# Optimization experiments

Measured on AMD Instinct MI355X. Metric: run time of the kernel, lower is better.

## Reference

```python
import jax, jax.numpy as jnp
import numpy as np
from jax import lax

HEAD_NUM = 16
QKV_DIM = 16
TOP_K = 2
SQRT_EMBED = 16.0   # sqrt_embedding_dim for E=256
LOGIT_CLIP = 10.0


def setup_inputs() -> dict:
    key = jax.random.key(0)
    ks = jax.random.split(key, 12)
    B, P, N1, E, HD, NE = 256, 100, 101, 256, 256, 8
    s = 0.05
    return {
        "encoded_last_node": jax.random.normal(ks[0], (B, P, E), jnp.float32),
        "attr": jax.random.uniform(ks[1], (B, P, 4), jnp.float32),
        "encoded_nodes": jax.random.normal(ks[2], (B, N1, E), jnp.float32),
        "ninf_mask": jnp.zeros((B, P, N1), jnp.float32),
        "attention_bias": jax.random.normal(ks[3], (B, P, N1), jnp.float32),
        "attention_bias1": jax.random.normal(ks[4], (B, P, N1), jnp.float32),
        "Wq_last": jax.random.normal(ks[5], (E + 4, HD), jnp.float32) * s,
        "Wk": jax.random.normal(ks[6], (E, HD), jnp.float32) * s,
        "Wv": jax.random.normal(ks[7], (E, HD), jnp.float32) * s,
        "Wg": jax.random.normal(ks[8], (HD, NE), jnp.float32) * s,
        "expert_W": jax.random.normal(ks[9], (NE, HD, E), jnp.float32) * s,
        "expert_b": jnp.zeros((NE, E), jnp.float32),
    }


def _heads(x, H, D):
    B, n, _ = x.shape
    return x.reshape(B, n, H, D).transpose(0, 2, 1, 3)  # (B,H,n,D)


def reference(encoded_last_node, attr, encoded_nodes, ninf_mask,
              attention_bias, attention_bias1, Wq_last, Wk, Wv,
              Wg, expert_W, expert_b):
    B, P, E = encoded_last_node.shape
    H, D = HEAD_NUM, QKV_DIM
    # q from [last_node ; attr], k/v from encoded_nodes (set_kv)
    q = _heads(jnp.concatenate([encoded_last_node, attr], axis=-1) @ Wq_last, H, D)
    k = _heads(encoded_nodes @ Wk, H, D)   # (B,H,N+1,D)
    v = _heads(encoded_nodes @ Wv, H, D)
    inv_sqrt_d = 1.0 / jnp.sqrt(jnp.asarray(D, jnp.float32))
    score = jnp.einsum('bhpd,bhnd->bhpn', q, k) * inv_sqrt_d
    score = score + ninf_mask[:, None, :, :]           # rank3 ninf mask
    w = jax.nn.softmax(score, axis=-1)
    out = jnp.einsum('bhpn,bhnd->bhpd', w, v)
    out_concat = out.transpose(0, 2, 1, 3).reshape(B, P, H * D)
    # --- top-k gated MoE combine (node-level routing, eval path) ---
    x = out_concat.reshape(B * P, H * D)               # tokens
    logits = x @ Wg                                    # (T, NE)
    top_v, top_i = lax.top_k(logits, TOP_K)
    top_g = jax.nn.softmax(top_v, axis=-1)
    gates = jnp.zeros_like(logits).at[
        jnp.arange(x.shape[0])[:, None], top_i].set(top_g)   # (T, NE)
    expert_out = jnp.einsum('tf,efo->teo', x, expert_W) + expert_b[None]
    mh = jnp.einsum('teo,te->to', expert_out, gates).reshape(B, P, E)
    # --- single-head pointer scores with bias + tanh clipping ---
    score2 = jnp.einsum('bpe,bne->bpn', mh, encoded_nodes)
    score2 = score2 + attention_bias + attention_bias1
    score2 = LOGIT_CLIP * jnp.tanh(score2 / SQRT_EMBED)
    probs = jax.nn.softmax(score2 + ninf_mask, axis=-1)  # (B,P,N+1)
    return probs
```

## Files before the change

kernel.cpp:

```cpp
#include <hip/hip_runtime.h>
#include <hip/hip_bf16.h>

#define B   256
#define P   100
#define N1  101
#define E   256
#define HD  256
#define H   16
#define D   16
#define NE  8
#define NTOK (B*P)
#define NKV  (B*N1)

typedef __attribute__((ext_vector_type(8))) short short8;
typedef __attribute__((ext_vector_type(4))) float f32x4;
typedef unsigned short ushort_t;

__device__ __forceinline__ unsigned short f2bf(float f) {
  unsigned int u = __float_as_uint(f);
  unsigned int r = (u + 0x7fffu + ((u >> 16) & 1u)) >> 16;
  return (unsigned short)r;
}
__device__ __forceinline__ float bf2f(unsigned short b) {
  return __uint_as_float(((unsigned int)b) << 16);
}
__device__ __forceinline__ unsigned int cvtpk(float a, float b) {
  unsigned int r;
  asm("v_cvt_pk_bf16_f32 %0, %1, %2" : "=v"(r) : "v"(a), "v"(b));
  return r;
}
__device__ __forceinline__ float lo2f(unsigned int u) {
  return __uint_as_float(u << 16);
}
__device__ __forceinline__ float hi2f(unsigned int u) {
  return __uint_as_float(u & 0xffff0000u);
}

__device__ __forceinline__ void split3_pack(const float* v, uint4& uh,
                                            uint4& um, uint4& ul) {
  unsigned int hw[4], mw[4], lw[4];
#pragma unroll
  for (int jj = 0; jj < 4; ++jj) {
    float va = v[2 * jj], vb = v[2 * jj + 1];
    unsigned int h = cvtpk(va, vb);
    float ra = va - lo2f(h), rb = vb - hi2f(h);
    unsigned int m = cvtpk(ra, rb);
    float sa = ra - lo2f(m), sb = rb - hi2f(m);
    unsigned int l = cvtpk(sa, sb);
    hw[jj] = h; mw[jj] = m; lw[jj] = l;
  }
  uh.x = hw[0]; uh.y = hw[1]; uh.z = hw[2]; uh.w = hw[3];
  um.x = mw[0]; um.y = mw[1]; um.z = mw[2]; um.w = mw[3];
  ul.x = lw[0]; ul.y = lw[1]; ul.z = lw[2]; ul.w = lw[3];
}

__global__ __launch_bounds__(256) void wsplit3_kernel(
    const float* __restrict__ W, uint4* __restrict__ Wp, int Kreal) {
  const int gid = blockIdx.x * 256 + threadIdx.x;
  const int lane = gid & 63;
  const int rest = gid >> 6;
  const int gct = rest & 15;
  const int kt = rest >> 4;
  const int k0 = kt * 32 + (lane >> 4) * 8;
  const int c = gct * 16 + (lane & 15);
  float v[8];
#pragma unroll
  for (int j = 0; j < 8; ++j) {
    int kk = k0 + j;
    v[j] = (kk < Kreal) ? W[(size_t)kk * 256 + c] : 0.f;
  }
  uint4 uh, um, ul;
  split3_pack(v, uh, um, ul);
  Wp[(size_t)(rest * 3 + 0) * 64 + lane] = uh;
  Wp[(size_t)(rest * 3 + 1) * 64 + lane] = um;
  Wp[(size_t)(rest * 3 + 2) * 64 + lane] = ul;
}

__global__ __launch_bounds__(256) void kvproj3_kernel(
    const float* __restrict__ enc, const uint4* __restrict__ Wk3,
    const uint4* __restrict__ Wv3, float* __restrict__ kout,
    float* __restrict__ vout) {
  const int KT = 8;
  const int NKG = KT * 4;
  const int RSTRIDE = KT * 12 + 1;
  __shared__ uint4 als[32 * 97];
  const int tid = threadIdx.x;
  const int row0 = blockIdx.x * 32;
  for (int i = tid; i < 32 * NKG; i += 256) {
    const int row = i >> 5;
    const int kg = i & 31;
    float v[8];
    const float4* s = (const float4*)(enc + (size_t)(row0 + row) * 256 + kg * 8);
    float4 x0 = s[0], x1 = s[1];
    v[0] = x0.x; v[1] = x0.y; v[2] = x0.z; v[3] = x0.w;
    v[4] = x1.x; v[5] = x1.y; v[6] = x1.z; v[7] = x1.w;
    uint4 uh, um, ul;
    split3_pack(v, uh, um, ul);
    const int slot = row * RSTRIDE + kg;
    als[slot] = uh;
    als[slot + NKG] = um;
    als[slot + 2 * NKG] = ul;
  }
  __syncthreads();
  const int w = tid >> 6;
  const int lane = tid & 63;
  const int lr = lane & 15;
  const int lg4 = lane >> 4;
  f32x4 acck[2][4], accv[2][4];
#pragma unroll
  for (int rt = 0; rt < 2; ++rt)
#pragma unroll
    for (int ct = 0; ct < 4; ++ct) {
      acck[rt][ct] = (f32x4){0.f, 0.f, 0.f, 0.f};
      accv[rt][ct] = (f32x4){0.f, 0.f, 0.f, 0.f};
    }
  for (int kt = 0; kt < KT; ++kt) {
    short8 ah[2], am[2], al[2];
#pragma unroll
    for (int rt = 0; rt < 2; ++rt) {
      const int base = (rt * 16 + lr) * RSTRIDE + kt * 4 + lg4;
      ah[rt] = __builtin_bit_cast(short8, als[base]);
      am[rt] = __builtin_bit_cast(short8, als[base + NKG]);
      al[rt] = __builtin_bit_cast(short8, als[base + 2 * NKG]);
    }
#pragma unroll
    for (int ct = 0; ct < 4; ++ct) {
      const int gct = w * 4 + ct;
      const size_t base = (size_t)((kt * 16 + gct) * 3) * 64 + lane;
      {
        short8 bh = __builtin_bit_cast(short8, Wk3[base]);
        short8 bm = __builtin_bit_cast(short8, Wk3[base + 64]);
        short8 bl = __builtin_bit_cast(short8, Wk3[base + 128]);
#pragma unroll
        for (int rt = 0; rt < 2; ++rt) {
          f32x4 a = acck[rt][ct];
          a = __builtin_amdgcn_mfma_f32_16x16x32_bf16(ah[rt], bh, a, 0, 0, 0);
          a = __builtin_amdgcn_mfma_f32_16x16x32_bf16(ah[rt], bm, a, 0, 0, 0);
          a = __builtin_amdgcn_mfma_f32_16x16x32_bf16(am[rt], bh, a, 0, 0, 0);
          a = __builtin_amdgcn_mfma_f32_16x16x32_bf16(am[rt], bm, a, 0, 0, 0);
          a = __builtin_amdgcn_mfma_f32_16x16x32_bf16(ah[rt], bl, a, 0, 0, 0);
          a = __builtin_amdgcn_mfma_f32_16x16x32_bf16(al[rt], bh, a, 0, 0, 0);
          acck[rt][ct] = a;
        }
      }
      {
        short8 bh = __builtin_bit_cast(short8, Wv3[base]);
        short8 bm = __builtin_bit_cast(short8, Wv3[base + 64]);
        short8 bl = __builtin_bit_cast(short8, Wv3[base + 128]);
#pragma unroll
        for (int rt = 0; rt < 2; ++rt) {
          f32x4 a = accv[rt][ct];
          a = __builtin_amdgcn_mfma_f32_16x16x32_bf16(ah[rt], bh, a, 0, 0, 0);
          a = __builtin_amdgcn_mfma_f32_16x16x32_bf16(ah[rt], bm, a, 0, 0, 0);
          a = __builtin_amdgcn_mfma_f32_16x16x32_bf16(am[rt], bh, a, 0, 0, 0);
          a = __builtin_amdgcn_mfma_f32_16x16x32_bf16(am[rt], bm, a, 0, 0, 0);
          a = __builtin_amdgcn_mfma_f32_16x16x32_bf16(ah[rt], bl, a, 0, 0, 0);
          a = __builtin_amdgcn_mfma_f32_16x16x32_bf16(al[rt], bh, a, 0, 0, 0);
          accv[rt][ct] = a;
        }
      }
    }
  }
#pragma unroll
  for (int rt = 0; rt < 2; ++rt) {
#pragma unroll
    for (int ct = 0; ct < 4; ++ct) {
      const int gct = w * 4 + ct;
#pragma unroll
      for (int reg = 0; reg < 4; ++reg) {
        const int row = row0 + rt * 16 + lg4 * 4 + reg;
        int bb = row / N1, nn = row - bb * N1;
        size_t o = (((size_t)bb * H + gct) * N1 + nn) * D + lr;
        kout[o] = acck[rt][ct][reg];
        vout[o] = accv[rt][ct][reg];
      }
    }
  }
}

template <int KT, int MODE>
__global__ __launch_bounds__(256) void proj3_kernel(
    const float* __restrict__ src, const float* __restrict__ attr,
    const uint4* __restrict__ Wp3, float* __restrict__ outp) {
  const int RSTRIDE = KT * 12 + 1;
  __shared__ uint4 als[32 * (KT * 12 + 1)];
  const int tid = threadIdx.x;
  const int row0 = blockIdx.x * 32;
  const int NKG = KT * 4;
  for (int i = tid; i < 32 * NKG; i += 256) {
    const int row = i / NKG;
    const int kg = i - row * NKG;
    float v[8];
    const int kbase = kg * 8;
    if (MODE == 0 || kbase < 256) {
      const float4* s = (const float4*)(src + (size_t)(row0 + row) * 256 + kbase);
      float4 x0 = s[0], x1 = s[1];
      v[0] = x0.x; v[1] = x0.y; v[2] = x0.z; v[3] = x0.w;
      v[4] = x1.x; v[5] = x1.y; v[6] = x1.z; v[7] = x1.w;
    } else {
#pragma unroll
      for (int j = 0; j < 8; ++j) {
        int k = kbase + j;
        v[j] = (k >= 256 && k < 260) ? attr[(size_t)(row0 + row) * 4 + (k - 256)]
                                     : 0.f;
      }
    }
    uint4 uh, um, ul;
    split3_pack(v, uh, um, ul);
    const int slot = row * RSTRIDE + kg;
    als[slot] = uh;
    als[slot + NKG] = um;
    als[slot + 2 * NKG] = ul;
  }
  __syncthreads();
  const int w = tid >> 6;
  const int lane = tid & 63;
  const int lr = lane & 15;
  const int lg4 = lane >> 4;
  f32x4 acc[2][4];
#pragma unroll
  for (int rt = 0; rt < 2; ++rt)
#pragma unroll
    for (int ct = 0; ct < 4; ++ct) acc[rt][ct] = (f32x4){0.f, 0.f, 0.f, 0.f};
  for (int kt = 0; kt < KT; ++kt) {
    short8 ah[2], am[2], al[2];
#pragma unroll
    for (int rt = 0; rt < 2; ++rt) {
      const int base = (rt * 16 + lr) * RSTRIDE + kt * 4 + lg4;
      ah[rt] = __builtin_bit_cast(short8, als[base]);
      am[rt] = __builtin_bit_cast(short8, als[base + NKG]);
      al[rt] = __builtin_bit_cast(short8, als[base + 2 * NKG]);
    }
#pragma unroll
    for (int ct = 0; ct < 4; ++ct) {
      const int gct = w * 4 + ct;
      const size_t base = (size_t)((kt * 16 + gct) * 3) * 64 + lane;
      short8 bh = __builtin_bit_cast(short8, Wp3[base]);
      short8 bm = __builtin_bit_cast(short8, Wp3[base + 64]);
      short8 bl = __builtin_bit_cast(short8, Wp3[base + 128]);
#pragma unroll
      for (int rt = 0; rt < 2; ++rt) {
        f32x4 a = acc[rt][ct];
        a = __builtin_amdgcn_mfma_f32_16x16x32_bf16(ah[rt], bh, a, 0, 0, 0);
        a = __builtin_amdgcn_mfma_f32_16x16x32_bf16(ah[rt], bm, a, 0, 0, 0);
        a = __builtin_amdgcn_mfma_f32_16x16x32_bf16(am[rt], bh, a, 0, 0, 0);
        a = __builtin_amdgcn_mfma_f32_16x16x32_bf16(am[rt], bm, a, 0, 0, 0);
        a = __builtin_amdgcn_mfma_f32_16x16x32_bf16(ah[rt], bl, a, 0, 0, 0);
        a = __builtin_amdgcn_mfma_f32_16x16x32_bf16(al[rt], bh, a, 0, 0, 0);
        acc[rt][ct] = a;
      }
    }
  }
#pragma unroll
  for (int rt = 0; rt < 2; ++rt) {
#pragma unroll
    for (int ct = 0; ct < 4; ++ct) {
      const int gct = w * 4 + ct;
#pragma unroll
      for (int reg = 0; reg < 4; ++reg) {
        const int row = row0 + rt * 16 + lg4 * 4 + reg;
        size_t o;
        if (MODE == 0) {
          int bb = row / N1, nn = row - bb * N1;
          o = (((size_t)bb * H + gct) * N1 + nn) * D + lr;
        } else {
          int bb = row / P, pp = row - bb * P;
          o = (((size_t)bb * H + gct) * P + pp) * D + lr;
        }
        outp[o] = acc[rt][ct][reg];
      }
    }
  }
}

__device__ __forceinline__ float dot16f(
    const float4& a0, const float4& a1, const float4& a2, const float4& a3,
    const float4& b0, const float4& b1, const float4& b2, const float4& b3) {
  float s = a0.x * b0.x;
  s = fmaf(a0.y, b0.y, s); s = fmaf(a0.z, b0.z, s); s = fmaf(a0.w, b0.w, s);
  s = fmaf(a1.x, b1.x, s); s = fmaf(a1.y, b1.y, s); s = fmaf(a1.z, b1.z, s);
  s = fmaf(a1.w, b1.w, s);
  s = fmaf(a2.x, b2.x, s); s = fmaf(a2.y, b2.y, s); s = fmaf(a2.z, b2.z, s);
  s = fmaf(a2.w, b2.w, s);
  s = fmaf(a3.x, b3.x, s); s = fmaf(a3.y, b3.y, s); s = fmaf(a3.z, b3.z, s);
  s = fmaf(a3.w, b3.w, s);
  return s;
}

__global__ __launch_bounds__(256) void attn_kernel(
    const float* __restrict__ q, const float* __restrict__ k,
    const float* __restrict__ v, const float* __restrict__ ninf,
    float* __restrict__ x) {
  const int b = blockIdx.x >> 3;
  const int h0 = (blockIdx.x & 7) * 2;
  __shared__ float4 kl4[2 * N1 * 4];
  __shared__ float4 vl4[2 * N1 * 4];
  const int tid = threadIdx.x;
  {
    const float4* ks = (const float4*)(k + ((size_t)b * H + h0) * N1 * D);
    const float4* vs = (const float4*)(v + ((size_t)b * H + h0) * N1 * D);
    for (int i = tid; i < 2 * N1 * 4; i += 256) {
      kl4[i] = ks[i];
      vl4[i] = vs[i];
    }
  }
  const int w = tid >> 6;
  const int lane = tid & 63;
  const int hh = w >> 1;
  const int h = h0 + hh;
  const int prow = (w & 1) * 64 + lane;
  const bool act = (prow < P);
  const int p = act ? prow : (P - 1);
  const float LOG2E = 1.4426950408889634f;
  const float c1 = 0.25f * LOG2E;
  const float* qb = q + (((size_t)b * H + h) * P + p) * D;
  float4 qa0 = *(const float4*)&qb[0];
  float4 qa1 = *(const float4*)&qb[4];
  float4 qa2 = *(const float4*)&qb[8];
  float4 qa3 = *(const float4*)&qb[12];
  qa0.x *= c1; qa0.y *= c1; qa0.z *= c1; qa0.w *= c1;
  qa1.x *= c1; qa1.y *= c1; qa1.z *= c1; qa1.w *= c1;
  qa2.x *= c1; qa2.y *= c1; qa2.z *= c1; qa2.w *= c1;
  qa3.x *= c1; qa3.y *= c1; qa3.z *= c1; qa3.w *= c1;
  const float* mrow = ninf + ((size_t)b * P + p) * N1;
  const float* kw = (const float*)(kl4 + hh * N1 * 4);
  const float* vw = (const float*)(vl4 + hh * N1 * 4);
  __syncthreads();

  float m2 = -1e30f, l = 0.f;
  float o[16];
#pragma unroll
  for (int d = 0; d < 16; ++d) o[d] = 0.f;
  float4 mk = *(const float4*)&mrow[0];
  const float tmask = mrow[100];

  for (int it = 0; it < 25; ++it) {
    const int j = it * 4;
    const int nn = (it < 24) ? (j + 4) : 0;
    float4 nx = *(const float4*)&mrow[nn];
    const float4* kr0 = (const float4*)&kw[(j + 0) * D];
    const float4* kr1 = (const float4*)&kw[(j + 1) * D];
    const float4* kr2 = (const float4*)&kw[(j + 2) * D];
    const float4* kr3 = (const float4*)&kw[(j + 3) * D];
    float4 k00 = kr0[0], k01 = kr0[1], k02 = kr0[2], k03 = kr0[3];
    float4 k10 = kr1[0], k11 = kr1[1], k12 = kr1[2], k13 = kr1[3];
    float4 k20 = kr2[0], k21 = kr2[1], k22 = kr2[2], k23 = kr2[3];
    float4 k30 = kr3[0], k31 = kr3[1], k32 = kr3[2], k33 = kr3[3];
    float s0 = fmaf(mk.x, LOG2E, dot16f(qa0, qa1, qa2, qa3, k00, k01, k02, k03));
    float s1 = fmaf(mk.y, LOG2E, dot16f(qa0, qa1, qa2, qa3, k10, k11, k12, k13));
    float s2 = fmaf(mk.z, LOG2E, dot16f(qa0, qa1, qa2, qa3, k20, k21, k22, k23));
    float s3 = fmaf(mk.w, LOG2E, dot16f(qa0, qa1, qa2, qa3, k30, k31, k32, k33));
    float mn = fmaxf(fmaxf(fmaxf(s0, s1), fmaxf(s2, s3)), m2);
    float sc = exp2f(m2 - mn);
    float p0 = exp2f(s0 - mn), p1 = exp2f(s1 - mn);
    float p2 = exp2f(s2 - mn), p3 = exp2f(s3 - mn);
    l = fmaf(l, sc, (p0 + p1) + (p2 + p3));
    const float4* vr0 = (const float4*)&vw[(j + 0) * D];
    const float4* vr1 = (const float4*)&vw[(j + 1) * D];
    const float4* vr2 = (const float4*)&vw[(j + 2) * D];
    const float4* vr3 = (const float4*)&vw[(j + 3) * D];
#pragma unroll
    for (int dq = 0; dq < 4; ++dq) {
      float4 v0 = vr0[dq], v1 = vr1[dq], v2 = vr2[dq], v3 = vr3[dq];
      o[4 * dq + 0] = fmaf(o[4 * dq + 0], sc,
          fmaf(p0, v0.x, fmaf(p1, v1.x, fmaf(p2, v2.x, p3 * v3.x))));
      o[4 * dq + 1] = fmaf(o[4 * dq + 1], sc,
          fmaf(p0, v0.y, fmaf(p1, v1.y, fmaf(p2, v2.y, p3 * v3.y))));
      o[4 * dq + 2] = fmaf(o[4 * dq + 2], sc,
          fmaf(p0, v0.z, fmaf(p1, v1.z, fmaf(p2, v2.z, p3 * v3.z))));
      o[4 * dq + 3] = fmaf(o[4 * dq + 3], sc,
          fmaf(p0, v0.w, fmaf(p1, v1.w, fmaf(p2, v2.w, p3 * v3.w))));
    }
    m2 = mn;
    mk = nx;
  }
  {
    const float4* kr = (const float4*)&kw[100 * D];
    float4 k0 = kr[0], k1 = kr[1], k2 = kr[2], k3 = kr[3];
    float s = fmaf(tmask, LOG2E, dot16f(qa0, qa1, qa2, qa3, k0, k1, k2, k3));
    float mn = fmaxf(m2, s);
    float sc = exp2f(m2 - mn);
    float pp = exp2f(s - mn);
    l = fmaf(l, sc, pp);
    const float4* vr = (const float4*)&vw[100 * D];
#pragma unroll
    for (int dq = 0; dq < 4; ++dq) {
      float4 v0 = vr[dq];
      o[4 * dq + 0] = fmaf(o[4 * dq + 0], sc, pp * v0.x);
      o[4 * dq + 1] = fmaf(o[4 * dq + 1], sc, pp * v0.y);
      o[4 * dq + 2] = fmaf(o[4 * dq + 2], sc, pp * v0.z);
      o[4 * dq + 3] = fmaf(o[4 * dq + 3], sc, pp * v0.w);
    }
  }
  if (act) {
    const float inv = 1.f / l;
    float* xr = &x[((size_t)b * P + p) * HD + h * D];
#pragma unroll
    for (int dq = 0; dq < 4; ++dq) {
      float4 t;
      t.x = o[4 * dq + 0] * inv; t.y = o[4 * dq + 1] * inv;
      t.z = o[4 * dq + 2] * inv; t.w = o[4 * dq + 3] * inv;
      *(float4*)&xr[4 * dq] = t;
    }
  }
}

__global__ __launch_bounds__(256) void logits_top2_kernel(
    const float* __restrict__ x, const float* __restrict__ Wg,
    int* __restrict__ topi, float* __restrict__ topg,
    ushort_t* __restrict__ xsplit) {
  __shared__ float xl[32][260];
  __shared__ float wg[E * NE];
  __shared__ float lg[32][9];
  const int tid = threadIdx.x;
  const int t0 = blockIdx.x * 32;
  for (int r = 0; r < 32; ++r) {
    float val = x[(size_t)(t0 + r) * HD + tid];
    xl[r][tid] = val;
    unsigned short hi = f2bf(val);
    unsigned short lo = f2bf(val - bf2f(hi));
    xsplit[(size_t)(t0 + r) * 512 + tid] = hi;
    xsplit[(size_t)(t0 + r) * 512 + 256 + tid] = lo;
  }
  for (int i = tid; i < E * NE; i += 256) wg[i] = Wg[i];
  __syncthreads();
  const int r = tid >> 3, e = tid & 7;
  float acc = 0.f;
  for (int f = 0; f < E; ++f) acc += xl[r][f] * wg[f * NE + e];
  lg[r][e] = acc;
  __syncthreads();
  if (tid < 32) {
    float v[8];
#pragma unroll
    for (int j = 0; j < 8; ++j) v[j] = lg[tid][j];
    int i1 = 0; float v1 = v[0];
#pragma unroll
    for (int j = 1; j < 8; ++j) if (v[j] > v1) { v1 = v[j]; i1 = j; }
    int i2 = -1; float v2 = -1e30f;
#pragma unroll
    for (int j = 0; j < 8; ++j)
      if (j != i1 && v[j] > v2) { v2 = v[j]; i2 = j; }
    float ex = __expf(v2 - v1);
    float g1 = 1.f / (1.f + ex);
    float g2 = ex / (1.f + ex);
    int t = t0 + tid;
    topi[t * 2 + 0] = i1; topi[t * 2 + 1] = i2;
    topg[t * 2 + 0] = g1; topg[t * 2 + 1] = g2;
  }
}

__global__ __launch_bounds__(1024) void build_lists_kernel(
    const int* __restrict__ topi, const float* __restrict__ topg,
    int* __restrict__ list_tok, float* __restrict__ list_gate,
    int* __restrict__ counts) {
  const int e = blockIdx.x;
  const int tid = threadIdx.x;
  const int lane = tid & 63, w = tid >> 6;
  __shared__ int wsum[16];
  int running = 0;
  for (int c = 0; c < NTOK; c += 1024) {
    int t = c + tid;
    int ia = topi[t * 2 + 0], ib = topi[t * 2 + 1];
    int slot = (ia == e) ? 0 : ((ib == e) ? 1 : -1);
    int f = (slot >= 0) ? 1 : 0;
    unsigned long long m = __ballot(f);
    if (lane == 0) wsum[w] = __popcll(m);
    __syncthreads();
    int wbase = 0, total = 0;
#pragma unroll
    for (int i = 0; i < 16; ++i) {
      int s = wsum[i];
      if (i < w) wbase += s;
      total += s;
    }
    if (f) {
      int prefix = __popcll(m & ((1ull << lane) - 1ull));
      int pos = running + wbase + prefix;
      list_tok[e * NTOK + pos] = (t << 1) | slot;
      list_gate[e * NTOK + pos] = topg[t * 2 + slot];
    }
    running += total;
    __syncthreads();
  }
  if (tid == 0) counts[e] = running;
}

__global__ __launch_bounds__(256) void wsplit_kernel(
    const float* __restrict__ eW, uint4* __restrict__ Wp) {
  const int gid = blockIdx.x * 256 + threadIdx.x;
  const int lane = gid & 63;
  const int rest = gid >> 6;
  const int gct = rest & 15;
  const int kt = (rest >> 4) & 7;
  const int e = rest >> 7;
  const int kbase = kt * 32 + (lane >> 4) * 8;
  const int c = gct * 16 + (lane & 15);
  unsigned int hi[4], lo[4];
#pragma unroll
  for (int jj = 0; jj < 4; ++jj) {
    float v0 = eW[((size_t)e * HD + (kbase + 2 * jj)) * E + c];
    float v1 = eW[((size_t)e * HD + (kbase + 2 * jj + 1)) * E + c];
    unsigned int h = cvtpk(v0, v1);
    float r0 = v0 - lo2f(h), r1 = v1 - hi2f(h);
    unsigned int l = cvtpk(r0, r1);
    hi[jj] = h; lo[jj] = l;
  }
  uint4 uh, ul;
  uh.x = hi[0]; uh.y = hi[1]; uh.z = hi[2]; uh.w = hi[3];
  ul.x = lo[0]; ul.y = lo[1]; ul.z = lo[2]; ul.w = lo[3];
  Wp[(size_t)(rest * 2 + 0) * 64 + lane] = uh;
  Wp[(size_t)(rest * 2 + 1) * 64 + lane] = ul;
}

__global__ __launch_bounds__(256) void expert_gemm_kernel(
    const ushort_t* __restrict__ xsplit, const uint4* __restrict__ Wp,
    const float* __restrict__ eb, const int* __restrict__ list_tok,
    const float* __restrict__ list_gate, const int* __restrict__ counts,
    float* __restrict__ p0, float* __restrict__ p1) {
  int e = 0, t0 = -1;
  {
    int rem = blockIdx.x;
    for (int i = 0; i < NE; ++i) {
      int nt = (counts[i] + 31) >> 5;
      if (rem < nt) { e = i; t0 = rem * 32; break; }
      rem -= nt;
    }
  }
  if (t0 < 0) return;
  const int cnt = counts[e];
  const int nr = min(32, cnt - t0);
  __shared__ uint4 xls[32 * 65];
  __shared__ int stok[32];
  __shared__ float sg[32];
  const int tid = threadIdx.x;
  if (tid < 32) {
    int src = e * NTOK + t0 + ((tid < nr) ? tid : 0);
    stok[tid] = list_tok[src];
    sg[tid] = (tid < nr) ? list_gate[e * NTOK + t0 + tid] : 0.f;
  }
  __syncthreads();
  for (int i = tid; i < 32 * 64; i += 256) {
    int r = i >> 6, ch = i & 63;
    const uint4* src = (const uint4*)(xsplit + (size_t)(stok[r] >> 1) * 512);
    xls[r * 65 + ch] = src[ch];
  }
  __syncthreads();
  const int w = tid >> 6;
  const int lane = tid & 63;
  const int lr = lane & 15;
  const int lg4 = lane >> 4;
  f32x4 acc[2][4];
#pragma unroll
  for (int rt = 0; rt < 2; ++rt)
#pragma unroll
    for (int ct = 0; ct < 4; ++ct) acc[rt][ct] = (f32x4){0.f, 0.f, 0.f, 0.f};

  for (int kt = 0; kt < 8; ++kt) {
    short8 afrag[2][2];
#pragma unroll
    for (int rt = 0; rt < 2; ++rt)
#pragma unroll
      for (int pl = 0; pl < 2; ++pl) {
        uint4 u = xls[(rt * 16 + lr) * 65 + pl * 32 + kt * 4 + lg4];
        afrag[rt][pl] = __builtin_bit_cast(short8, u);
      }
#pragma unroll
    for (int ct = 0; ct < 4; ++ct) {
      const int gct = w * 4 + ct;
      const size_t base = (size_t)(((e * 8 + kt) * 16 + gct) * 2) * 64 + lane;
      short8 bh = __builtin_bit_cast(short8, Wp[base]);
      short8 bl = __builtin_bit_cast(short8, Wp[base + 64]);
#pragma unroll
      for (int rt = 0; rt < 2; ++rt) {
        acc[rt][ct] = __builtin_amdgcn_mfma_f32_16x16x32_bf16(
            afrag[rt][0], bh, acc[rt][ct], 0, 0, 0);
        acc[rt][ct] = __builtin_amdgcn_mfma_f32_16x16x32_bf16(
            afrag[rt][0], bl, acc[rt][ct], 0, 0, 0);
        acc[rt][ct] = __builtin_amdgcn_mfma_f32_16x16x32_bf16(
            afrag[rt][1], bh, acc[rt][ct], 0, 0, 0);
      }
    }
  }
#pragma unroll
  for (int rt = 0; rt < 2; ++rt) {
#pragma unroll
    for (int ct = 0; ct < 4; ++ct) {
      const int col = (w * 4 + ct) * 16 + lr;
      const float bias = eb[e * E + col];
#pragma unroll
      for (int reg = 0; reg < 4; ++reg) {
        const int ridx = rt * 16 + lg4 * 4 + reg;
        if (ridx < nr) {
          const int tokw = stok[ridx];
          const float g = sg[ridx];
          float* dst = ((tokw & 1) ? p1 : p0) + (size_t)(tokw >> 1) * E + col;
          *dst = g * (acc[rt][ct][reg] + bias);
        }
      }
    }
  }
}

__global__ __launch_bounds__(128) void score2_kernel(
    const float* __restrict__ p0, const float* __restrict__ p1,
    const float* __restrict__ enc, float* __restrict__ out) {
  const int b = blockIdx.y;
  const int pt = blockIdx.x * 25;
  __shared__ float mh[25][E];
  const int tid = threadIdx.x;
  for (int i = tid; i < 25 * E; i += 128) {
    int r = i >> 8, c = i & 255;
    int t = b * P + pt + r;
    mh[r][c] = p0[(size_t)t * E + c] + p1[(size_t)t * E + c];
  }
  __syncthreads();
  const int n = tid;
  if (n >= N1) return;
  float acc[25];
#pragma unroll
  for (int r = 0; r < 25; ++r) acc[r] = 0.f;
  const float* er = enc + ((size_t)b * N1 + n) * E;
  for (int ee = 0; ee < E; ee += 4) {
    float4 ev = *(const float4*)&er[ee];
#pragma unroll
    for (int r = 0; r < 25; ++r) {
      float4 mv = *(const float4*)&mh[r][ee];
      acc[r] += mv.x * ev.x + mv.y * ev.y + mv.z * ev.z + mv.w * ev.w;
    }
  }
#pragma unroll
  for (int r = 0; r < 25; ++r) out[((size_t)b * P + pt + r) * N1 + n] = acc[r];
}

__global__ __launch_bounds__(256) void softmax2_kernel(
    float* __restrict__ sc, const float* __restrict__ ab,
    const float* __restrict__ ab1, const float* __restrict__ ninf) {
  const int row = blockIdx.x * 4 + (threadIdx.x >> 6);
  const int lane = threadIdx.x & 63;
  float* srow = sc + (size_t)row * N1;
  const float* a = ab + (size_t)row * N1;
  const float* a1 = ab1 + (size_t)row * N1;
  const float* nf = ninf + (size_t)row * N1;
  float s0 = -1e30f, s1 = -1e30f;
  {
    int i = lane;
    float s = srow[i] + a[i] + a1[i];
    float e2 = __expf(s * 0.125f);
    float th = 1.f - 2.f / (e2 + 1.f);
    s0 = 10.f * th + nf[i];
  }
  if (lane < N1 - 64) {
    int i = lane + 64;
    float s = srow[i] + a[i] + a1[i];
    float e2 = __expf(s * 0.125f);
    float th = 1.f - 2.f / (e2 + 1.f);
    s1 = 10.f * th + nf[i];
  }
  float mx = fmaxf(s0, s1);
#pragma unroll
  for (int off = 32; off > 0; off >>= 1) mx = fmaxf(mx, __shfl_xor(mx, off, 64));
  float p0 = __expf(s0 - mx);
  float p1 = (lane < N1 - 64) ? __expf(s1 - mx) : 0.f;
  float sum = p0 + p1;
#pragma unroll
  for (int off = 32; off > 0; off >>= 1) sum += __shfl_xor(sum, off, 64);
  float inv = 1.f / sum;
  srow[lane] = p0 * inv;
  if (lane < N1 - 64) srow[lane + 64] = p1 * inv;
}

extern "C" void kernel_launch(void* const* d_in, const int* in_sizes, int n_in,
                              void* d_out, int out_size, void* d_ws,
                              size_t ws_size, hipStream_t stream) {
  const float* eln  = (const float*)d_in[0];
  const float* attr = (const float*)d_in[1];
  const float* enc  = (const float*)d_in[2];
  const float* ninf = (const float*)d_in[3];
  const float* ab   = (const float*)d_in[4];
  const float* ab1  = (const float*)d_in[5];
  const float* Wq   = (const float*)d_in[6];
  const float* Wk   = (const float*)d_in[7];
  const float* Wv   = (const float*)d_in[8];
  const float* Wg   = (const float*)d_in[9];
  const float* eW   = (const float*)d_in[10];
  const float* eb   = (const float*)d_in[11];
  float* out = (float*)d_out;

  char* ws = (char*)d_ws;
  size_t off = 0;
  auto carve = [&](size_t bytes) {
    char* p = ws + off;
    off += (bytes + 255) & ~size_t(255);
    return p;
  };
  float* kbuf = (float*)carve(sizeof(float) * NKV * HD);
  float* vbuf = (float*)carve(sizeof(float) * NKV * HD);
  float* qbuf = (float*)carve(sizeof(float) * NTOK * HD);
  float* xbuf = (float*)carve(sizeof(float) * NTOK * HD);
  int*   topi = (int*)carve(sizeof(int) * NTOK * 2);
  float* topg = (float*)carve(sizeof(float) * NTOK * 2);
  int*   counts = (int*)carve(sizeof(int) * 16);
  int*   list_tok = (int*)carve(sizeof(int) * NE * NTOK);
  float* list_gate = (float*)carve(sizeof(float) * NE * NTOK);
  uint4* Wp  = (uint4*)carve(sizeof(ushort_t) * NE * HD * E * 2);
  uint4* Wk3 = (uint4*)carve((size_t)8 * 16 * 3 * 64 * 16);
  uint4* Wv3 = (uint4*)carve((size_t)8 * 16 * 3 * 64 * 16);
  uint4* Wq3 = (uint4*)carve((size_t)9 * 16 * 3 * 64 * 16);
  float* pp0 = kbuf;
  float* pp1 = vbuf;
  ushort_t* xsplit = (ushort_t*)qbuf;

  wsplit_kernel<<<256, 256, 0, stream>>>(eW, Wp);
  wsplit3_kernel<<<32, 256, 0, stream>>>(Wk, Wk3, 256);
  wsplit3_kernel<<<32, 256, 0, stream>>>(Wv, Wv3, 256);
  wsplit3_kernel<<<36, 256, 0, stream>>>(Wq, Wq3, 260);
  kvproj3_kernel<<<NKV / 32, 256, 0, stream>>>(enc, Wk3, Wv3, kbuf, vbuf);
  proj3_kernel<9, 1><<<NTOK / 32, 256, 0, stream>>>(eln, attr, Wq3, qbuf);
  attn_kernel<<<B * 8, 256, 0, stream>>>(qbuf, kbuf, vbuf, ninf, xbuf);
  logits_top2_kernel<<<NTOK / 32, 256, 0, stream>>>(xbuf, Wg, topi, topg,
                                                    xsplit);
  build_lists_kernel<<<NE, 1024, 0, stream>>>(topi, topg, list_tok, list_gate,
                                              counts);
  expert_gemm_kernel<<<1608, 256, 0, stream>>>(xsplit, Wp, eb, list_tok,
                                               list_gate, counts, pp0, pp1);
  dim3 s2(4, B);
  score2_kernel<<<s2, 128, 0, stream>>>(pp0, pp1, enc, out);
  softmax2_kernel<<<NTOK / 4, 256, 0, stream>>>(out, ab, ab1, ninf);
}
```

Before: 328.3 us.

## Fuse score2 with softmax, chunk attention K/V staging, enlarge expert GEMM tiles

Merges the pointer-score GEMM with the bias, tanh-clip and softmax stage into one kernel, so the score matrix is no longer written and re-read from global memory. The attention kernel now stages K/V into shared memory in two chunks, which lowers LDS use per block and may allow higher occupancy, at the cost of extra barriers. The expert GEMM tile grows from 32 to 48 tokens per block with a matching grid size, trading more registers and LDS per block for fewer blocks and more reuse of each weight load.

```diff
diff --git a/kernel.cpp b/kernel.cpp
--- a/kernel.cpp
+++ b/kernel.cpp
@@ -293,17 +293,9 @@
     float* __restrict__ x) {
   const int b = blockIdx.x >> 3;
   const int h0 = (blockIdx.x & 7) * 2;
-  __shared__ float4 kl4[2 * N1 * 4];
-  __shared__ float4 vl4[2 * N1 * 4];
+  __shared__ float4 kl4[2 * 208];
+  __shared__ float4 vl4[2 * 208];
   const int tid = threadIdx.x;
-  {
-    const float4* ks = (const float4*)(k + ((size_t)b * H + h0) * N1 * D);
-    const float4* vs = (const float4*)(v + ((size_t)b * H + h0) * N1 * D);
-    for (int i = tid; i < 2 * N1 * 4; i += 256) {
-      kl4[i] = ks[i];
-      vl4[i] = vs[i];
-    }
-  }
   const int w = tid >> 6;
   const int lane = tid & 63;
   const int hh = w >> 1;
@@ -323,66 +315,83 @@
   qa2.x *= c1; qa2.y *= c1; qa2.z *= c1; qa2.w *= c1;
   qa3.x *= c1; qa3.y *= c1; qa3.z *= c1; qa3.w *= c1;
   const float* mrow = ninf + ((size_t)b * P + p) * N1;
-  const float* kw = (const float*)(kl4 + hh * N1 * 4);
-  const float* vw = (const float*)(vl4 + hh * N1 * 4);
-  __syncthreads();
+  const float* kw = (const float*)(kl4 + hh * 208);
+  const float* vw = (const float*)(vl4 + hh * 208);
 
   float m2 = -1e30f, l = 0.f;
   float o[16];
 #pragma unroll
   for (int d = 0; d < 16; ++d) o[d] = 0.f;
-  float4 mk = *(const float4*)&mrow[0];
-  const float tmask = mrow[100];
-
-  for (int it = 0; it < 25; ++it) {
-    const int j = it * 4;
-    const int nn = (it < 24) ? (j + 4) : 0;
-    float4 nx = *(const float4*)&mrow[nn];
-    const float4* kr0 = (const float4*)&kw[(j + 0) * D];
-    const float4* kr1 = (const float4*)&kw[(j + 1) * D];
-    const float4* kr2 = (const float4*)&kw[(j + 2) * D];
-    const float4* kr3 = (const float4*)&kw[(j + 3) * D];
-    float4 k00 = kr0[0], k01 = kr0[1], k02 = kr0[2], k03 = kr0[3];
-    float4 k10 = kr1[0], k11 = kr1[1], k12 = kr1[2], k13 = kr1[3];
-    float4 k20 = kr2[0], k21 = kr2[1], k22 = kr2[2], k23 = kr2[3];
-    float4 k30 = kr3[0], k31 = kr3[1], k32 = kr3[2], k33 = kr3[3];
-    float s0 = fmaf(mk.x, LOG2E, dot16f(qa0, qa1, qa2, qa3, k00, k01, k02, k03));
-    float s1 = fmaf(mk.y, LOG2E, dot16f(qa0, qa1, qa2, qa3, k10, k11, k12, k13));
-    float s2 = fmaf(mk.z, LOG2E, dot16f(qa0, qa1, qa2, qa3, k20, k21, k22, k23));
-    float s3 = fmaf(mk.w, LOG2E, dot16f(qa0, qa1, qa2, qa3, k30, k31, k32, k33));
-    float mn = fmaxf(fmaxf(fmaxf(s0, s1), fmaxf(s2, s3)), m2);
-    float sc = exp2f(m2 - mn);
-    float p0 = exp2f(s0 - mn), p1 = exp2f(s1 - mn);
-    float p2 = exp2f(s2 - mn), p3 = exp2f(s3 - mn);
-    l = fmaf(l, sc, (p0 + p1) + (p2 + p3));
-    const float4* vr0 = (const float4*)&vw[(j + 0) * D];
-    const float4* vr1 = (const float4*)&vw[(j + 1) * D];
-    const float4* vr2 = (const float4*)&vw[(j + 2) * D];
-    const float4* vr3 = (const float4*)&vw[(j + 3) * D];
-#pragma unroll
-    for (int dq = 0; dq < 4; ++dq) {
-      float4 v0 = vr0[dq], v1 = vr1[dq], v2 = vr2[dq], v3 = vr3[dq];
-      o[4 * dq + 0] = fmaf(o[4 * dq + 0], sc,
-          fmaf(p0, v0.x, fmaf(p1, v1.x, fmaf(p2, v2.x, p3 * v3.x))));
-      o[4 * dq + 1] = fmaf(o[4 * dq + 1], sc,
-          fmaf(p0, v0.y, fmaf(p1, v1.y, fmaf(p2, v2.y, p3 * v3.y))));
-      o[4 * dq + 2] = fmaf(o[4 * dq + 2], sc,
-          fmaf(p0, v0.z, fmaf(p1, v1.z, fmaf(p2, v2.z, p3 * v3.z))));
-      o[4 * dq + 3] = fmaf(o[4 * dq + 3], sc,
-          fmaf(p0, v0.w, fmaf(p1, v1.w, fmaf(p2, v2.w, p3 * v3.w))));
-    }
-    m2 = mn;
-    mk = nx;
+
+#pragma unroll
+  for (int ch = 0; ch < 2; ++ch) {
+    const int c0 = ch ? 52 : 0;
+    const int len = ch ? 49 : 52;
+    const int nf4 = len * 4;
+    __syncthreads();
+    for (int i = tid; i < 2 * nf4; i += 256) {
+      int hs = i / nf4, rem = i - hs * nf4;
+      const float4* ks =
+          (const float4*)(k + (((size_t)b * H + h0 + hs) * N1 + c0) * D);
+      const float4* vs =
+          (const float4*)(v + (((size_t)b * H + h0 + hs) * N1 + c0) * D);
+      kl4[hs * 208 + rem] = ks[rem];
+      vl4[hs * 208 + rem] = vs[rem];
+    }
+    __syncthreads();
+    const int nit = len >> 2;
+    float4 mk = *(const float4*)&mrow[c0];
+    for (int it = 0; it < nit; ++it) {
+      const int j = it * 4;
+      const int nn = (it < nit - 1) ? (c0 + j + 4) : c0;
+      float4 nx = *(const float4*)&mrow[nn];
+      const float4* kr0 = (const float4*)&kw[(j + 0) * D];
+      const float4* kr1 = (const float4*)&kw[(j + 1) * D];
+      const float4* kr2 = (const float4*)&kw[(j + 2) * D];
+      const float4* kr3 = (const float4*)&kw[(j + 3) * D];
+      float4 k00 = kr0[0], k01 = kr0[1], k02 = kr0[2], k03 = kr0[3];
+      float4 k10 = kr1[0], k11 = kr1[1], k12 = kr1[2], k13 = kr1[3];
+      float4 k20 = kr2[0], k21 = kr2[1], k22 = kr2[2], k23 = kr2[3];
+      float4 k30 = kr3[0], k31 = kr3[1], k32 = kr3[2], k33 = kr3[3];
+      float s0 = fmaf(mk.x, LOG2E, dot16f(qa0, qa1, qa2, qa3, k00, k01, k02, k03));
+      float s1 = fmaf(mk.y, LOG2E, dot16f(qa0, qa1, qa2, qa3, k10, k11, k12, k13));
+      float s2 = fmaf(mk.z, LOG2E, dot16f(qa0, qa1, qa2, qa3, k20, k21, k22, k23));
+      float s3 = fmaf(mk.w, LOG2E, dot16f(qa0, qa1, qa2, qa3, k30, k31, k32, k33));
+      float mn = fmaxf(fmaxf(fmaxf(s0, s1), fmaxf(s2, s3)), m2);
+      float sc = exp2f(m2 - mn);
+      float p0 = exp2f(s0 - mn), p1 = exp2f(s1 - mn);
+      float p2 = exp2f(s2 - mn), p3 = exp2f(s3 - mn);
+      l = fmaf(l, sc, (p0 + p1) + (p2 + p3));
+      const float4* vr0 = (const float4*)&vw[(j + 0) * D];
+      const float4* vr1 = (const float4*)&vw[(j + 1) * D];
+      const float4* vr2 = (const float4*)&vw[(j + 2) * D];
+      const float4* vr3 = (const float4*)&vw[(j + 3) * D];
+#pragma unroll
+      for (int dq = 0; dq < 4; ++dq) {
+        float4 v0 = vr0[dq], v1 = vr1[dq], v2 = vr2[dq], v3 = vr3[dq];
+        o[4 * dq + 0] = fmaf(o[4 * dq + 0], sc,
+            fmaf(p0, v0.x, fmaf(p1, v1.x, fmaf(p2, v2.x, p3 * v3.x))));
+        o[4 * dq + 1] = fmaf(o[4 * dq + 1], sc,
+            fmaf(p0, v0.y, fmaf(p1, v1.y, fmaf(p2, v2.y, p3 * v3.y))));
+        o[4 * dq + 2] = fmaf(o[4 * dq + 2], sc,
+            fmaf(p0, v0.z, fmaf(p1, v1.z, fmaf(p2, v2.z, p3 * v3.z))));
+        o[4 * dq + 3] = fmaf(o[4 * dq + 3], sc,
+            fmaf(p0, v0.w, fmaf(p1, v1.w, fmaf(p2, v2.w, p3 * v3.w))));
+      }
+      m2 = mn;
+      mk = nx;
+    }
   }
   {
-    const float4* kr = (const float4*)&kw[100 * D];
+    const float tm = mrow[100];
+    const float4* kr = (const float4*)&kw[48 * D];
     float4 k0 = kr[0], k1 = kr[1], k2 = kr[2], k3 = kr[3];
-    float s = fmaf(tmask, LOG2E, dot16f(qa0, qa1, qa2, qa3, k0, k1, k2, k3));
+    float s = fmaf(tm, LOG2E, dot16f(qa0, qa1, qa2, qa3, k0, k1, k2, k3));
     float mn = fmaxf(m2, s);
     float sc = exp2f(m2 - mn);
     float pp = exp2f(s - mn);
     l = fmaf(l, sc, pp);
-    const float4* vr = (const float4*)&vw[100 * D];
+    const float4* vr = (const float4*)&vw[48 * D];
 #pragma unroll
     for (int dq = 0; dq < 4; ++dq) {
       float4 v0 = vr[dq];
@@ -521,25 +530,25 @@
   {
     int rem = blockIdx.x;
     for (int i = 0; i < NE; ++i) {
-      int nt = (counts[i] + 31) >> 5;
-      if (rem < nt) { e = i; t0 = rem * 32; break; }
+      int nt = (counts[i] + 47) / 48;
+      if (rem < nt) { e = i; t0 = rem * 48; break; }
       rem -= nt;
     }
   }
   if (t0 < 0) return;
   const int cnt = counts[e];
-  const int nr = min(32, cnt - t0);
-  __shared__ uint4 xls[32 * 65];
-  __shared__ int stok[32];
-  __shared__ float sg[32];
+  const int nr = min(48, cnt - t0);
+  __shared__ uint4 xls[48 * 65];
+  __shared__ int stok[48];
+  __shared__ float sg[48];
   const int tid = threadIdx.x;
-  if (tid < 32) {
+  if (tid < 48) {
     int src = e * NTOK + t0 + ((tid < nr) ? tid : 0);
     stok[tid] = list_tok[src];
     sg[tid] = (tid < nr) ? list_gate[e * NTOK + t0 + tid] : 0.f;
   }
   __syncthreads();
-  for (int i = tid; i < 32 * 64; i += 256) {
+  for (int i = tid; i < 48 * 64; i += 256) {
     int r = i >> 6, ch = i & 63;
     const uint4* src = (const uint4*)(xsplit + (size_t)(stok[r] >> 1) * 512);
     xls[r * 65 + ch] = src[ch];
@@ -549,16 +558,16 @@
   const int lane = tid & 63;
   const int lr = lane & 15;
   const int lg4 = lane >> 4;
-  f32x4 acc[2][4];
-#pragma unroll
-  for (int rt = 0; rt < 2; ++rt)
+  f32x4 acc[3][4];
+#pragma unroll
+  for (int rt = 0; rt < 3; ++rt)
 #pragma unroll
     for (int ct = 0; ct < 4; ++ct) acc[rt][ct] = (f32x4){0.f, 0.f, 0.f, 0.f};
 
   for (int kt = 0; kt < 8; ++kt) {
-    short8 afrag[2][2];
-#pragma unroll
-    for (int rt = 0; rt < 2; ++rt)
+    short8 afrag[3][2];
+#pragma unroll
+    for (int rt = 0; rt < 3; ++rt)
 #pragma unroll
       for (int pl = 0; pl < 2; ++pl) {
         uint4 u = xls[(rt * 16 + lr) * 65 + pl * 32 + kt * 4 + lg4];
@@ -571,7 +580,7 @@
       short8 bh = __builtin_bit_cast(short8, Wp[base]);
       short8 bl = __builtin_bit_cast(short8, Wp[base + 64]);
 #pragma unroll
-      for (int rt = 0; rt < 2; ++rt) {
+      for (int rt = 0; rt < 3; ++rt) {
         acc[rt][ct] = __builtin_amdgcn_mfma_f32_16x16x32_bf16(
             afrag[rt][0], bh, acc[rt][ct], 0, 0, 0);
         acc[rt][ct] = __builtin_amdgcn_mfma_f32_16x16x32_bf16(
@@ -582,7 +591,7 @@
     }
   }
 #pragma unroll
-  for (int rt = 0; rt < 2; ++rt) {
+  for (int rt = 0; rt < 3; ++rt) {
 #pragma unroll
     for (int ct = 0; ct < 4; ++ct) {
       const int col = (w * 4 + ct) * 16 + lr;
@@ -601,72 +610,85 @@
   }
 }
 
-__global__ __launch_bounds__(128) void score2_kernel(
+__global__ __launch_bounds__(256) void score2_fused_kernel(
     const float* __restrict__ p0, const float* __restrict__ p1,
-    const float* __restrict__ enc, float* __restrict__ out) {
-  const int b = blockIdx.y;
-  const int pt = blockIdx.x * 25;
-  __shared__ float mh[25][E];
+    const float* __restrict__ enc, const float* __restrict__ ab,
+    const float* __restrict__ ab1, const float* __restrict__ ninf,
+    float* __restrict__ out) {
+  const int b = blockIdx.x >> 1;
+  const int half = blockIdx.x & 1;
+  const int r0 = half * 50;
+  __shared__ float4 mh4[50 * 64];
   const int tid = threadIdx.x;
-  for (int i = tid; i < 25 * E; i += 128) {
-    int r = i >> 8, c = i & 255;
-    int t = b * P + pt + r;
-    mh[r][c] = p0[(size_t)t * E + c] + p1[(size_t)t * E + c];
+  for (int i = tid; i < 50 * 64; i += 256) {
+    int r = i >> 6, c4 = i & 63;
+    size_t idx = (size_t)(b * P + r0 + r) * 64 + c4;
+    float4 a = ((const float4*)p0)[idx];
+    float4 c = ((const float4*)p1)[idx];
+    float4 s;
+    s.x = a.x + c.x; s.y = a.y + c.y; s.z = a.z + c.z; s.w = a.w + c.w;
+    mh4[i] = s;
   }
   __syncthreads();
-  const int n = tid;
-  if (n >= N1) return;
-  float acc[25];
-#pragma unroll
-  for (int r = 0; r < 25; ++r) acc[r] = 0.f;
-  const float* er = enc + ((size_t)b * N1 + n) * E;
-  for (int ee = 0; ee < E; ee += 4) {
-    float4 ev = *(const float4*)&er[ee];
-#pragma unroll
-    for (int r = 0; r < 25; ++r) {
-      float4 mv = *(const float4*)&mh[r][ee];
-      acc[r] += mv.x * ev.x + mv.y * ev.y + mv.z * ev.z + mv.w * ev.w;
-    }
-  }
-#pragma unroll
-  for (int r = 0; r < 25; ++r) out[((size_t)b * P + pt + r) * N1 + n] = acc[r];
-}
-
-__global__ __launch_bounds__(256) void softmax2_kernel(
-    float* __restrict__ sc, const float* __restrict__ ab,
-    const float* __restrict__ ab1, const float* __restrict__ ninf) {
-  const int row = blockIdx.x * 4 + (threadIdx.x >> 6);
-  const int lane = threadIdx.x & 63;
-  float* srow = sc + (size_t)row * N1;
-  const float* a = ab + (size_t)row * N1;
-  const float* a1 = ab1 + (size_t)row * N1;
-  const float* nf = ninf + (size_t)row * N1;
-  float s0 = -1e30f, s1 = -1e30f;
-  {
-    int i = lane;
-    float s = srow[i] + a[i] + a1[i];
-    float e2 = __expf(s * 0.125f);
-    float th = 1.f - 2.f / (e2 + 1.f);
-    s0 = 10.f * th + nf[i];
-  }
-  if (lane < N1 - 64) {
-    int i = lane + 64;
-    float s = srow[i] + a[i] + a1[i];
-    float e2 = __expf(s * 0.125f);
-    float th = 1.f - 2.f / (e2 + 1.f);
-    s1 = 10.f * th + nf[i];
-  }
-  float mx = fmaxf(s0, s1);
-#pragma unroll
-  for (int off = 32; off > 0; off >>= 1) mx = fmaxf(mx, __shfl_xor(mx, off, 64));
-  float p0 = __expf(s0 - mx);
-  float p1 = (lane < N1 - 64) ? __expf(s1 - mx) : 0.f;
-  float sum = p0 + p1;
-#pragma unroll
-  for (int off = 32; off > 0; off >>= 1) sum += __shfl_xor(sum, off, 64);
-  float inv = 1.f / sum;
-  srow[lane] = p0 * inv;
-  if (lane < N1 - 64) srow[lane + 64] = p1 * inv;
+  const int w = tid >> 6;
+  const int lane = tid & 63;
+  const int n0 = lane;
+  const int n1v = lane + 64;
+  const bool has1 = (n1v < N1);
+  const int n1 = has1 ? n1v : (N1 - 1);
+  const float4* er0 = (const float4*)(enc + ((size_t)b * N1 + n0) * E);
+  const float4* er1 = (const float4*)(enc + ((size_t)b * N1 + n1) * E);
+  float acc0[13], acc1[13];
+#pragma unroll
+  for (int j = 0; j < 13; ++j) { acc0[j] = 0.f; acc1[j] = 0.f; }
+  for (int kk = 0; kk < 64; ++kk) {
+    float4 e0 = er0[kk];
+    float4 e1 = er1[kk];
+#pragma unroll
+    for (int j = 0; j < 13; ++j) {
+      const int r = w + j * 4;
+      if (r < 50) {
+        float4 mv = mh4[r * 64 + kk];
+        acc0[j] = fmaf(mv.w, e0.w,
+                  fmaf(mv.z, e0.z, fmaf(mv.y, e0.y, fmaf(mv.x, e0.x, acc0[j]))));
+        acc1[j] = fmaf(mv.w, e1.w,
+                  fmaf(mv.z, e1.z, fmaf(mv.y, e1.y, fmaf(mv.x, e1.x, acc1[j]))));
+      }
+    }
+  }
+#pragma unroll
+  for (int j = 0; j < 13; ++j) {
+    const int r = w + j * 4;
+    if (r < 50) {
+      const int prow = b * P + r0 + r;
+      const float* arow = ab + (size_t)prow * N1;
+      const float* a1row = ab1 + (size_t)prow * N1;
+      const float* nrow = ninf + (size_t)prow * N1;
+      float s0 = acc0[j] + arow[n0] + a1row[n0];
+      float e20 = __expf(s0 * 0.125f);
+      float v0 = 10.f - 20.f / (e20 + 1.f) + nrow[n0];
+      float v1 = -1e30f;
+      if (has1) {
+        float s1 = acc1[j] + arow[n1v] + a1row[n1v];
+        float e21 = __expf(s1 * 0.125f);
+        v1 = 10.f - 20.f / (e21 + 1.f) + nrow[n1v];
+      }
+      float mx = fmaxf(v0, v1);
+#pragma unroll
+      for (int off = 32; off > 0; off >>= 1)
+        mx = fmaxf(mx, __shfl_xor(mx, off, 64));
+      float q0 = __expf(v0 - mx);
+      float q1 = has1 ? __expf(v1 - mx) : 0.f;
+      float sum = q0 + q1;
+#pragma unroll
+      for (int off = 32; off > 0; off >>= 1)
+        sum += __shfl_xor(sum, off, 64);
+      float inv = 1.f / sum;
+      float* orow = out + (size_t)prow * N1;
+      orow[n0] = q0 * inv;
+      if (has1) orow[n1v] = q1 * inv;
+    }
+  }
 }
 
 extern "C" void kernel_launch(void* const* d_in, const int* in_sizes, int n_in,
@@ -721,9 +743,8 @@
                                                     xsplit);
   build_lists_kernel<<<NE, 1024, 0, stream>>>(topi, topg, list_tok, list_gate,
                                               counts);
-  expert_gemm_kernel<<<1608, 256, 0, stream>>>(xsplit, Wp, eb, list_tok,
+  expert_gemm_kernel<<<1075, 256, 0, stream>>>(xsplit, Wp, eb, list_tok,
                                                list_gate, counts, pp0, pp1);
-  dim3 s2(4, B);
-  score2_kernel<<<s2, 128, 0, stream>>>(pp0, pp1, enc, out);
-  softmax2_kernel<<<NTOK / 4, 256, 0, stream>>>(out, ab, ab1, ninf);
-}
+  score2_fused_kernel<<<512, 256, 0, stream>>>(pp0, pp1, enc, ab, ab1, ninf,
+                                               out);
+}
```

Result: faster. 319.0 us (-2.8%).
